# Kernel tuning notes

Measured on AMD Instinct MI355X. Metric: run time of the kernel, lower is better.

The kernel has to match this reference:

```python
import jax, jax.numpy as jnp
import numpy as np

N_NODES = 100000
N_EDGES = 1600000
D_IN = 512
D_HID = 128
N_CLASSES = 100


def _gcn_norm(edge_index, n_nodes):
    # Add self loops and compute symmetric normalization D^{-1/2} (A+I) D^{-1/2}
    sl = jnp.arange(n_nodes, dtype=edge_index.dtype)
    src = jnp.concatenate([edge_index[0], sl])
    dst = jnp.concatenate([edge_index[1], sl])
    deg = jax.ops.segment_sum(jnp.ones_like(dst, dtype=jnp.float32), dst,
                              num_segments=n_nodes)
    dinv = jnp.where(deg > 0, jax.lax.rsqrt(deg), 0.0)
    norm = dinv[src] * dinv[dst]  # [E + N]
    return src, dst, norm


def _gcn_layer(x, W, b, src, dst, norm, n_nodes):
    h = x @ W                                  # [N, d_out] (transform first, like PyG GCNConv)
    msg = h[src] * norm[:, None]               # [E+N, d_out] gather + scale
    out = jax.ops.segment_sum(msg, dst, num_segments=n_nodes)  # scatter-add
    return out + b


def setup_inputs() -> dict:
    key = jax.random.key(0)
    ks = jax.random.split(key, 6)
    x = jax.random.normal(ks[0], (N_NODES, D_IN), dtype=jnp.float32)
    edge_index = jax.random.randint(ks[1], (2, N_EDGES), 0, N_NODES, dtype=jnp.int64)
    W1 = jax.random.normal(ks[2], (D_IN, D_HID), dtype=jnp.float32) * (1.0 / np.sqrt(D_IN))
    b1 = jnp.zeros((D_HID,), dtype=jnp.float32)
    W2 = jax.random.normal(ks[3], (D_HID, N_CLASSES), dtype=jnp.float32) * (1.0 / np.sqrt(D_HID))
    b2 = jnp.zeros((N_CLASSES,), dtype=jnp.float32)
    return {"x": x, "edge_index": edge_index, "W1": W1, "b1": b1, "W2": W2, "b2": b2}


def reference(x, edge_index, W1, b1, W2, b2):
    n_nodes = x.shape[0]
    src, dst, norm = _gcn_norm(edge_index, n_nodes)
    h = jax.nn.relu(_gcn_layer(x, W1, b1, src, dst, norm, n_nodes))
    logits = _gcn_layer(h, W2, b2, src, dst, norm, n_nodes)
    return jax.nn.log_softmax(logits, axis=-1)
```

## Files before the change

### kernel.cpp

```cpp
#include <hip/hip_runtime.h>
#include <math.h>

typedef __attribute__((ext_vector_type(8))) short short8;
typedef __attribute__((ext_vector_type(4))) float f32x4;
typedef _Float16 half8 __attribute__((ext_vector_type(8)));
typedef __fp16 fp16x2 __attribute__((ext_vector_type(2)));
typedef unsigned int uint;

__device__ inline uint f2bf(float f) {
    uint u = __float_as_uint(f);
    return (u + 0x7fffu + ((u >> 16) & 1u)) >> 16;
}
__device__ inline uint pack2(float lo, float hi) { return f2bf(lo) | (f2bf(hi) << 16); }
__device__ inline float bflo(uint u) { return __uint_as_float(u << 16); }
__device__ inline float bfhi(uint u) { return __uint_as_float(u & 0xffff0000u); }
__device__ inline uint cvtpk(float lo, float hi) {
    uint r;
    asm("v_cvt_pk_bf16_f32 %0, %1, %2" : "=v"(r) : "v"(lo), "v"(hi));
    return r;
}
__device__ inline uint pkh(float lo, float hi) {
    union { fp16x2 h; uint u; } c;
    c.h = __builtin_amdgcn_cvt_pkrtz(lo, hi);
    return c.u;
}
__device__ inline void gload16(const void* g, void* l) {
    __builtin_amdgcn_global_load_lds(
        (const __attribute__((address_space(1))) void*)g,
        (__attribute__((address_space(3))) void*)l, 16, 0, 0);
}

__global__ void k_degree(const int* __restrict__ dst, int E, int* __restrict__ cnt) {
    int i = blockIdx.x * 256 + threadIdx.x;
    if (i < E) atomicAdd(&cnt[dst[i]], 1);
}

__global__ void k_dinv(const int* __restrict__ cnt, float* __restrict__ dinv, int N) {
    int i = blockIdx.x * 256 + threadIdx.x;
    if (i < N) dinv[i] = rsqrtf((float)(cnt[i] + 1));
}

__global__ __launch_bounds__(512) void k_scan1(const int* __restrict__ cnt, int* __restrict__ rp,
                                               int* __restrict__ partials, int N) {
    __shared__ int s[512];
    int i = blockIdx.x * 512 + threadIdx.x;
    int v = (i < N) ? cnt[i] : 0;
    s[threadIdx.x] = v;
    __syncthreads();
    for (int d = 1; d < 512; d <<= 1) {
        int t = (threadIdx.x >= d) ? s[threadIdx.x - d] : 0;
        __syncthreads();
        s[threadIdx.x] += t;
        __syncthreads();
    }
    if (i < N) rp[i] = s[threadIdx.x] - v;
    if (threadIdx.x == 511) partials[blockIdx.x] = s[511];
}

__global__ void k_scan2(int* __restrict__ partials, int nb) {
    if (threadIdx.x == 0 && blockIdx.x == 0) {
        int acc = 0;
        for (int i = 0; i < nb; i++) { int v = partials[i]; partials[i] = acc; acc += v; }
    }
}

__global__ __launch_bounds__(512) void k_scan3(int* __restrict__ rp, const int* __restrict__ partials,
                                               int N, int E) {
    int i = blockIdx.x * 512 + threadIdx.x;
    if (i < N) rp[i] += partials[blockIdx.x];
    if (i == 0) rp[N] = E;
}

__global__ void k_fill(const int* __restrict__ src, const int* __restrict__ dst, int E,
                       const int* __restrict__ rp, int* __restrict__ cursor,
                       const float* __restrict__ dinv, float2* __restrict__ colw) {
    int i = blockIdx.x * 256 + threadIdx.x;
    if (i < E) {
        int d = dst[i];
        int s = src[i];
        int pos = rp[d] + atomicAdd(&cursor[d], 1);
        colw[pos] = make_float2(__int_as_float(s), dinv[s]);
    }
}

__global__ void k_w1prep(const float* __restrict__ W1, ushort* __restrict__ frag) {
    int tid = blockIdx.x * 256 + threadIdx.x;
    if (tid < 8192) {
        int ks = tid >> 9;
        int t = (tid >> 6) & 7;
        int l = tid & 63;
        int kbase = ks * 32 + (l >> 4) * 8;
        int c = t * 16 + (l & 15);
#pragma unroll
        for (int j = 0; j < 8; j++) {
            float v = W1[(size_t)(kbase + j) * 128 + c];
            union { _Float16 h; ushort u; } cv;
            cv.h = (_Float16)v;
            frag[(size_t)tid * 8 + j] = cv.u;
        }
    }
}

__global__ __launch_bounds__(256) void k_gemm1(const float* __restrict__ x,
                                               const uint4* __restrict__ w1f,
                                               uint* __restrict__ h1, int N) {
    __shared__ char lds[131072];
    int tid = threadIdx.x, wv = tid >> 6, l = tid & 63;
    int cl = l & 15, kg = l >> 4;
    int row0 = blockIdx.x * 64;

    auto stage = [&](int c) {
        char* xbase = lds + (c & 1) * 32768;
        char* bbase = lds + 65536 + (c & 1) * 32768;
        const char* bsrc = (const char*)w1f + (size_t)(c * 2048) * 16;
#pragma unroll
        for (int i = 0; i < 8; i++) {
            int s = wv * 512 + i * 64 + l;
            int row = s >> 5, kk = s & 31;
            int kslot = kk ^ (row & 7);
            int rg = row0 + row; if (rg >= N) rg = N - 1;
            const float* gs = x + (size_t)rg * 512 + c * 128 + kslot * 4;
            gload16(gs, xbase + (size_t)(s - l) * 16);
            gload16(bsrc + (size_t)s * 16, bbase + (size_t)(s - l) * 16);
        }
    };

    f32x4 acc[8];
#pragma unroll
    for (int t = 0; t < 8; t++) acc[t] = (f32x4){0.f, 0.f, 0.f, 0.f};

    union U { uint4 u4; half8 h8; };
    int rowl = wv * 16 + cl;
    int swz = cl & 7;

    stage(0);
    __syncthreads();
    for (int c = 0; c < 4; c++) {
        if (c < 3) stage(c + 1);
        const char* xbase = lds + (c & 1) * 32768;
        const char* bbase = lds + 65536 + (c & 1) * 32768;
#pragma unroll
        for (int ks = 0; ks < 4; ks++) {
            int k4 = ks * 8 + kg * 2;
            float4 a0 = *(const float4*)(xbase + (size_t)(rowl * 32 + (k4 ^ swz)) * 16);
            float4 a1 = *(const float4*)(xbase + (size_t)(rowl * 32 + ((k4 + 1) ^ swz)) * 16);
            U A;
            A.u4.x = pkh(a0.x, a0.y);
            A.u4.y = pkh(a0.z, a0.w);
            A.u4.z = pkh(a1.x, a1.y);
            A.u4.w = pkh(a1.z, a1.w);
#pragma unroll
            for (int t = 0; t < 8; t++) {
                U B;
                B.u4 = *(const uint4*)(bbase + (size_t)(((ks * 8 + t) * 64 + l)) * 16);
                acc[t] = __builtin_amdgcn_mfma_f32_16x16x32_f16(A.h8, B.h8, acc[t], 0, 0, 0);
            }
        }
        if (c < 3) __syncthreads();
    }

    uint* hsp = (uint*)lds;
#pragma unroll
    for (int t = 0; t < 8; t++)
#pragma unroll
        for (int r = 0; r < 4; r++) {
            float mine = acc[t][r];
            float other = __shfl_xor(mine, 1, 64);
            if ((cl & 1) == 0)
                hsp[(wv * 16 + kg * 4 + r) * 66 + t * 8 + (cl >> 1)] = cvtpk(mine, other);
        }
#pragma unroll
    for (int it = 0; it < 16; it++) {
        int gr = row0 + wv * 16 + it;
        if (gr < N) h1[(size_t)gr * 64 + l] = hsp[(wv * 16 + it) * 66 + l];
    }
}

template <bool RELU_BIAS>
__global__ __launch_bounds__(256) void k_agg(const uint* __restrict__ h, const float* __restrict__ dinv,
                                             const int* __restrict__ rp, const float2* __restrict__ colw,
                                             const float* __restrict__ bias, uint* __restrict__ outb, int N) {
    int wave = threadIdx.x >> 6, lane = threadIdx.x & 63;
    int v = blockIdx.x * 4 + wave;
    if (v >= N) return;
    float dv = dinv[v];
    float wself = dv * dv;
    uint us = h[(size_t)v * 64 + lane];
    float acc0 = bflo(us) * wself;
    float acc1 = bfhi(us) * wself;
    int e0 = rp[v], e1 = rp[v + 1];
    int i = e0;
    for (; i + 8 <= e1; i += 8) {
        float2 q[8];
        uint u[8];
#pragma unroll
        for (int j = 0; j < 8; j++) q[j] = colw[i + j];
#pragma unroll
        for (int j = 0; j < 8; j++) u[j] = h[(size_t)__float_as_int(q[j].x) * 64 + lane];
#pragma unroll
        for (int j = 0; j < 8; j++) {
            float w = q[j].y * dv;
            acc0 = fmaf(bflo(u[j]), w, acc0);
            acc1 = fmaf(bfhi(u[j]), w, acc1);
        }
    }
    if (i + 4 <= e1) {
        float2 q[4];
        uint u[4];
#pragma unroll
        for (int j = 0; j < 4; j++) q[j] = colw[i + j];
#pragma unroll
        for (int j = 0; j < 4; j++) u[j] = h[(size_t)__float_as_int(q[j].x) * 64 + lane];
#pragma unroll
        for (int j = 0; j < 4; j++) {
            float w = q[j].y * dv;
            acc0 = fmaf(bflo(u[j]), w, acc0);
            acc1 = fmaf(bfhi(u[j]), w, acc1);
        }
        i += 4;
    }
    for (; i < e1; i++) {
        float2 q = colw[i];
        uint u = h[(size_t)__float_as_int(q.x) * 64 + lane];
        float w = q.y * dv;
        acc0 = fmaf(bflo(u), w, acc0);
        acc1 = fmaf(bfhi(u), w, acc1);
    }
    if (RELU_BIAS) {
        float2 b = *(const float2*)&bias[2 * lane];
        acc0 = fmaxf(acc0 + b.x, 0.f);
        acc1 = fmaxf(acc1 + b.y, 0.f);
    }
    outb[(size_t)v * 64 + lane] = pack2(acc0, acc1);
}

__global__ void k_w2prep(const float* __restrict__ W2, const float* __restrict__ b2,
                         ushort* __restrict__ frag, float* __restrict__ b2pad) {
    int tid = blockIdx.x * 256 + threadIdx.x;
    if (tid < 1792) {
        int q = tid / 448;
        int t = (tid >> 6) % 7;
        int l = tid & 63;
        int kbase = q * 32 + (l >> 4) * 8;
        int c = t * 16 + (l & 15);
#pragma unroll
        for (int j = 0; j < 8; j++) {
            float v = (c < 100) ? W2[(kbase + j) * 100 + c] : 0.f;
            frag[(size_t)tid * 8 + j] = (ushort)f2bf(v);
        }
    } else if (tid < 1792 + 112) {
        int c = tid - 1792;
        b2pad[c] = (c < 100) ? b2[c] : -1e30f;
    }
}

__global__ __launch_bounds__(256) void k_out_mfma(const uint* __restrict__ g2u,
                                                  const uint4* __restrict__ w2fragG,
                                                  const float* __restrict__ b2pad,
                                                  float* __restrict__ out, int N) {
    __shared__ uint4 w2s[1792];
    __shared__ float b2s[112];
    int tid = threadIdx.x;
    for (int i = tid; i < 1792; i += 256) w2s[i] = w2fragG[i];
    if (tid < 112) b2s[tid] = b2pad[tid];
    __syncthreads();

    int w = tid >> 6, l = tid & 63;
    int v0 = blockIdx.x * 128 + w * 32;
    int cl = l & 15, gq = l >> 4;

    f32x4 acc[2][7];
#pragma unroll
    for (int m = 0; m < 2; m++)
#pragma unroll
        for (int t = 0; t < 7; t++) acc[m][t] = (f32x4){0.f, 0.f, 0.f, 0.f};

    union U { uint4 u4; short8 s8; };

#pragma unroll
    for (int q = 0; q < 4; q++) {
        short8 afr[2];
#pragma unroll
        for (int m = 0; m < 2; m++) {
            int rv = v0 + m * 16 + cl;
            if (rv >= N) rv = N - 1;
            U a;
            a.u4 = *(const uint4*)&g2u[(size_t)rv * 64 + q * 16 + gq * 4];
            afr[m] = a.s8;
        }
#pragma unroll
        for (int t = 0; t < 7; t++) {
            U b;
            b.u4 = w2s[(q * 7 + t) * 64 + l];
            acc[0][t] = __builtin_amdgcn_mfma_f32_16x16x32_bf16(afr[0], b.s8, acc[0][t], 0, 0, 0);
            acc[1][t] = __builtin_amdgcn_mfma_f32_16x16x32_bf16(afr[1], b.s8, acc[1][t], 0, 0, 0);
        }
    }

    float bsv[7];
#pragma unroll
    for (int t = 0; t < 7; t++) bsv[t] = b2s[t * 16 + cl];

#pragma unroll
    for (int m = 0; m < 2; m++) {
#pragma unroll
        for (int r = 0; r < 4; r++) {
            int row = v0 + m * 16 + gq * 4 + r;
            float lg[7];
#pragma unroll
            for (int t = 0; t < 7; t++) lg[t] = acc[m][t][r] + bsv[t];
            float mx = lg[0];
#pragma unroll
            for (int t = 1; t < 7; t++) mx = fmaxf(mx, lg[t]);
            mx = fmaxf(mx, __shfl_xor(mx, 1, 64));
            mx = fmaxf(mx, __shfl_xor(mx, 2, 64));
            mx = fmaxf(mx, __shfl_xor(mx, 4, 64));
            mx = fmaxf(mx, __shfl_xor(mx, 8, 64));
            float s = 0.f;
#pragma unroll
            for (int t = 0; t < 7; t++) s += __expf(lg[t] - mx);
            s += __shfl_xor(s, 1, 64);
            s += __shfl_xor(s, 2, 64);
            s += __shfl_xor(s, 4, 64);
            s += __shfl_xor(s, 8, 64);
            float lse = mx + __logf(s);
            if (row < N) {
#pragma unroll
                for (int t = 0; t < 7; t++) {
                    int c = t * 16 + cl;
                    if (c < 100) out[(size_t)row * 100 + c] = lg[t] - lse;
                }
            }
        }
    }
}

extern "C" void kernel_launch(void* const* d_in, const int* in_sizes, int n_in,
                              void* d_out, int out_size, void* d_ws, size_t ws_size,
                              hipStream_t stream) {
    const float* x  = (const float*)d_in[0];
    const int*   ei = (const int*)d_in[1];
    const float* W1 = (const float*)d_in[2];
    const float* b1 = (const float*)d_in[3];
    const float* W2 = (const float*)d_in[4];
    const float* b2 = (const float*)d_in[5];
    float* out = (float*)d_out;

    int N = in_sizes[0] / 512;
    int E = in_sizes[1] / 2;
    const int* srcI = ei;
    const int* dstI = ei + E;

    char* wsb = (char*)d_ws;
    size_t off = 0;
    auto alloc = [&](size_t bytes) {
        void* p = wsb + off;
        off = (off + bytes + 255) & ~(size_t)255;
        return p;
    };
    int*    cnt      = (int*)alloc((size_t)N * 4);
    int*    cursor   = (int*)alloc((size_t)N * 4);
    float*  dinv     = (float*)alloc((size_t)N * 4);
    int*    rp       = (int*)alloc((size_t)(N + 1) * 4);
    int*    partials = (int*)alloc(1024 * 4);
    ushort* w1f      = (ushort*)alloc(8192 * 8 * 2);
    ushort* w2frag   = (ushort*)alloc(1792 * 8 * 2);
    float*  b2pad    = (float*)alloc(112 * 4);
    float2* colw     = (float2*)alloc((size_t)E * 8);
    uint*   h1       = (uint*)alloc((size_t)N * 64 * 4);
    uint*   a1       = (uint*)alloc((size_t)N * 64 * 4);
    uint*   g2       = h1;

    hipMemsetAsync(cnt, 0, (size_t)N * 4, stream);
    hipMemsetAsync(cursor, 0, (size_t)N * 4, stream);

    k_degree<<<(E + 255) / 256, 256, 0, stream>>>(dstI, E, cnt);
    k_dinv<<<(N + 255) / 256, 256, 0, stream>>>(cnt, dinv, N);
    int nb = (N + 511) / 512;
    k_scan1<<<nb, 512, 0, stream>>>(cnt, rp, partials, N);
    k_scan2<<<1, 64, 0, stream>>>(partials, nb);
    k_scan3<<<nb, 512, 0, stream>>>(rp, partials, N, E);
    k_fill<<<(E + 255) / 256, 256, 0, stream>>>(srcI, dstI, E, rp, cursor, dinv, colw);
    k_w1prep<<<32, 256, 0, stream>>>(W1, w1f);
    k_w2prep<<<8, 256, 0, stream>>>(W2, b2, w2frag, b2pad);

    k_gemm1<<<(N + 63) / 64, 256, 0, stream>>>(x, (const uint4*)w1f, h1, N);
    k_agg<true><<<(N + 3) / 4, 256, 0, stream>>>(h1, dinv, rp, colw, b1, a1, N);
    k_agg<false><<<(N + 3) / 4, 256, 0, stream>>>(a1, dinv, rp, colw, nullptr, g2, N);
    k_out_mfma<<<(N + 127) / 128, 256, 0, stream>>>(g2, (const uint4*)w2frag, b2pad, out, N);
}
```

Before: 425.1 us.

## Restructure gemm1 to 32-row tiles with fp16 X staged once in LDS

The first-layer GEMM now processes 32 rows per block instead of 64. Each block loads its whole X tile into registers up front, converts it to fp16, and stores it swizzled in LDS. Only W1 fragments are double-buffered over 8 k-chunks, and the four waves split the work as 2 row halves by 2 column halves. This halves LDS use to 64 KB so more blocks can be resident, and it converts X once rather than on each fragment read. The cost is that W1 is reloaded by twice as many blocks, there are more barriers, and the large register array for X may raise register pressure.

Result: no change. 432.2 us (+1.7%).

```diff
diff --git a/kernel.cpp b/kernel.cpp
--- a/kernel.cpp
+++ b/kernel.cpp
@@ -104,75 +104,84 @@
 __global__ __launch_bounds__(256) void k_gemm1(const float* __restrict__ x,
                                                const uint4* __restrict__ w1f,
                                                uint* __restrict__ h1, int N) {
-    __shared__ char lds[131072];
+    __shared__ char lds[65536];
     int tid = threadIdx.x, wv = tid >> 6, l = tid & 63;
     int cl = l & 15, kg = l >> 4;
-    int row0 = blockIdx.x * 64;
-
-    auto stage = [&](int c) {
-        char* xbase = lds + (c & 1) * 32768;
-        char* bbase = lds + 65536 + (c & 1) * 32768;
-        const char* bsrc = (const char*)w1f + (size_t)(c * 2048) * 16;
-#pragma unroll
-        for (int i = 0; i < 8; i++) {
-            int s = wv * 512 + i * 64 + l;
-            int row = s >> 5, kk = s & 31;
-            int kslot = kk ^ (row & 7);
-            int rg = row0 + row; if (rg >= N) rg = N - 1;
-            const float* gs = x + (size_t)rg * 512 + c * 128 + kslot * 4;
-            gload16(gs, xbase + (size_t)(s - l) * 16);
+    int row0 = blockIdx.x * 32;
+    int rhalf = wv & 1, chalf = wv >> 1;
+
+    auto stageB = [&](int c) {
+        char* bbase = lds + 32768 + (c & 1) * 16384;
+        const char* bsrc = (const char*)w1f + (size_t)c * 16384;
+#pragma unroll
+        for (int i = 0; i < 4; i++) {
+            int s = i * 256 + tid;
             gload16(bsrc + (size_t)s * 16, bbase + (size_t)(s - l) * 16);
         }
     };
 
-    f32x4 acc[8];
-#pragma unroll
-    for (int t = 0; t < 8; t++) acc[t] = (f32x4){0.f, 0.f, 0.f, 0.f};
+    float4 xa[16];
+#pragma unroll
+    for (int p = 0; p < 16; p++) {
+        int g4 = p * 256 + tid;
+        int r = g4 >> 7;
+        int rg = row0 + r; if (rg >= N) rg = N - 1;
+        xa[p] = *(const float4*)(x + (size_t)rg * 512 + (size_t)(g4 & 127) * 4);
+    }
+    stageB(0);
+#pragma unroll
+    for (int p = 0; p < 16; p++) {
+        int g4 = p * 256 + tid;
+        int r = g4 >> 7;
+        int f = g4 & 127;
+        uint lo = pkh(xa[p].x, xa[p].y);
+        uint hi = pkh(xa[p].z, xa[p].w);
+        int gran = (f >> 1) ^ (r & 7);
+        *(uint2*)(lds + (size_t)r * 1024 + gran * 16 + (f & 1) * 8) = make_uint2(lo, hi);
+    }
+    __syncthreads();
+
+    f32x4 acc[4];
+#pragma unroll
+    for (int t = 0; t < 4; t++) acc[t] = (f32x4){0.f, 0.f, 0.f, 0.f};
 
     union U { uint4 u4; half8 h8; };
-    int rowl = wv * 16 + cl;
-    int swz = cl & 7;
-
-    stage(0);
-    __syncthreads();
-    for (int c = 0; c < 4; c++) {
-        if (c < 3) stage(c + 1);
-        const char* xbase = lds + (c & 1) * 32768;
-        const char* bbase = lds + 65536 + (c & 1) * 32768;
-#pragma unroll
-        for (int ks = 0; ks < 4; ks++) {
-            int k4 = ks * 8 + kg * 2;
-            float4 a0 = *(const float4*)(xbase + (size_t)(rowl * 32 + (k4 ^ swz)) * 16);
-            float4 a1 = *(const float4*)(xbase + (size_t)(rowl * 32 + ((k4 + 1) ^ swz)) * 16);
+    int arow = rhalf * 16 + cl;
+
+    for (int c = 0; c < 8; c++) {
+        if (c < 7) stageB(c + 1);
+        const char* bb = lds + 32768 + (c & 1) * 16384;
+#pragma unroll
+        for (int k2 = 0; k2 < 2; k2++) {
+            int ks = c * 2 + k2;
+            int slot = (ks * 4 + kg) ^ (arow & 7);
             U A;
-            A.u4.x = pkh(a0.x, a0.y);
-            A.u4.y = pkh(a0.z, a0.w);
-            A.u4.z = pkh(a1.x, a1.y);
-            A.u4.w = pkh(a1.z, a1.w);
-#pragma unroll
-            for (int t = 0; t < 8; t++) {
+            A.u4 = *(const uint4*)(lds + (size_t)arow * 1024 + slot * 16);
+#pragma unroll
+            for (int tt = 0; tt < 4; tt++) {
                 U B;
-                B.u4 = *(const uint4*)(bbase + (size_t)(((ks * 8 + t) * 64 + l)) * 16);
-                acc[t] = __builtin_amdgcn_mfma_f32_16x16x32_f16(A.h8, B.h8, acc[t], 0, 0, 0);
+                B.u4 = *(const uint4*)(bb + (size_t)(((k2 * 8 + chalf * 4 + tt) * 64 + l)) * 16);
+                acc[tt] = __builtin_amdgcn_mfma_f32_16x16x32_f16(A.h8, B.h8, acc[tt], 0, 0, 0);
             }
         }
-        if (c < 3) __syncthreads();
-    }
-
-    uint* hsp = (uint*)lds;
-#pragma unroll
-    for (int t = 0; t < 8; t++)
+        __syncthreads();
+    }
+
+    uint* hsp = (uint*)lds + (size_t)wv * (16 * 33);
+#pragma unroll
+    for (int tt = 0; tt < 4; tt++)
 #pragma unroll
         for (int r = 0; r < 4; r++) {
-            float mine = acc[t][r];
+            float mine = acc[tt][r];
             float other = __shfl_xor(mine, 1, 64);
             if ((cl & 1) == 0)
-                hsp[(wv * 16 + kg * 4 + r) * 66 + t * 8 + (cl >> 1)] = cvtpk(mine, other);
-        }
-#pragma unroll
-    for (int it = 0; it < 16; it++) {
-        int gr = row0 + wv * 16 + it;
-        if (gr < N) h1[(size_t)gr * 64 + l] = hsp[(wv * 16 + it) * 66 + l];
+                hsp[(kg * 4 + r) * 33 + tt * 8 + (cl >> 1)] = cvtpk(mine, other);
+        }
+#pragma unroll
+    for (int p = 0; p < 8; p++) {
+        int it = p * 2 + (l >> 5);
+        int gr = row0 + rhalf * 16 + it;
+        if (gr < N) h1[(size_t)gr * 64 + chalf * 32 + (l & 31)] = hsp[it * 33 + (l & 31)];
     }
 }
 
@@ -384,7 +393,7 @@
     k_w1prep<<<32, 256, 0, stream>>>(W1, w1f);
     k_w2prep<<<8, 256, 0, stream>>>(W2, b2, w2frag, b2pad);
 
-    k_gemm1<<<(N + 63) / 64, 256, 0, stream>>>(x, (const uint4*)w1f, h1, N);
+    k_gemm1<<<(N + 31) / 32, 256, 0, stream>>>(x, (const uint4*)w1f, h1, N);
     k_agg<true><<<(N + 3) / 4, 256, 0, stream>>>(h1, dinv, rp, colw, b1, a1, N);
     k_agg<false><<<(N + 3) / 4, 256, 0, stream>>>(a1, dinv, rp, colw, nullptr, g2, N);
     k_out_mfma<<<(N + 127) / 128, 256, 0, stream>>>(g2, (const uint4*)w2frag, b2pad, out, N);
```
